# Optimization experiments

Hardware: AMD Instinct MI355X
Metric: run time of the kernel (lower is better)

Reference implementation:

```python
import jax, jax.numpy as jnp
import numpy as np

DT = 0.1       # integration step (ms)
TAU_M = 10.0   # membrane time constant
TAU_S = 5.0    # synaptic time constant
E_REV = 1.0    # synaptic reversal potential
G_MAX = 1.0    # synaptic conductance scale
P, N, E, B, T = 8, 2048, 16, 4, 128


def setup_inputs() -> dict:
    key = jax.random.key(0)
    k_src, k_tgt, k_w, k_win = jax.random.split(key, 4)
    t_seq = jnp.arange(B * T, dtype=jnp.float32).reshape(B, T) * DT  # [B,T] times in ms
    src = jax.random.randint(k_src, (E,), 0, P, dtype=jnp.int32)
    tgt = jax.random.randint(k_tgt, (E,), 0, P, dtype=jnp.int32)
    W = jax.random.normal(k_w, (E, N, N), jnp.float32) * (1.0 / np.sqrt(N))
    W_in = jax.random.normal(k_win, (N, N), jnp.float32) * (1.0 / np.sqrt(N))
    v0 = jnp.zeros((P, B, N), jnp.float32)      # population states
    s0 = jnp.zeros((E, B, N), jnp.float32)      # recurrent synapse states
    s_in0 = jnp.zeros((B, N), jnp.float32)      # input synapse state
    return dict(t_seq=t_seq, W=W, W_in=W_in, v0=v0, s0=s0, s_in0=s_in0, src=src, tgt=tgt)


def _input_rate(t, n):
    # InputPopulation: firing rate is a pure function of time t, per-unit phase.
    phase = jnp.arange(n, dtype=jnp.float32) * (2.0 * jnp.pi / n)
    return 0.5 * (1.0 + jnp.sin(2.0 * jnp.pi * t[:, None] / 100.0 + phase[None, :]))  # [B,n]


def _simulate(t_seq, W, W_in, v0, s0, s_in0, src, tgt):
    n_pop = v0.shape[0]

    def step(carry, t):  # t: [B] current time
        v, s, s_in, err = carry
        rates = jax.nn.sigmoid(v)                      # [P,B,N] firing rates
        # --- synapse message passing: gather pre rates, dense projection ---
        pre = rates[src]                               # [E,B,N]
        drive = jnp.einsum('ebi,eij->ebj', pre, W)     # [E,B,N]
        s_new = s + DT * (-s / TAU_S + drive)          # exponential synapse state
        # --- input population synapse (pre rate is a function of t) ---
        rate_in = _input_rate(t, v.shape[-1])          # [B,N]
        s_in_new = s_in + DT * (-s_in / TAU_S + rate_in @ W_in)
        # --- conductance-based currents scattered into target populations ---
        post_v = v[tgt]                                # [E,B,N]
        I_e = G_MAX * s_new * (E_REV - post_v)
        g_e = G_MAX * s_new
        I_sum = jax.ops.segment_sum(I_e, tgt, num_segments=n_pop)  # [P,B,N]
        g_sum = jax.ops.segment_sum(g_e, tgt, num_segments=n_pop)
        I_in = G_MAX * s_in_new * (E_REV - v[0])
        I_sum = I_sum.at[0].add(I_in)
        g_sum = g_sum.at[0].add(G_MAX * s_in_new)
        # --- Euler integrator step + stability error accumulation ---
        dv = (-v - g_sum * v + I_sum) / TAU_M
        v_new = v + DT * dv
        err_new = err + jnp.mean(jnp.abs(dv)) * DT
        return (v_new, s_new, s_in_new, err_new), jax.nn.sigmoid(v_new)

    init = (v0, s0, s_in0, jnp.zeros((), jnp.float32))
    (v_f, s_f, s_in_f, err), rates_seq = jax.lax.scan(step, init, t_seq.T)  # rates_seq: [T,P,B,N]
    firing_rates = jnp.transpose(rates_seq, (2, 0, 1, 3))  # [B,T,P,N]
    return firing_rates, err


def reference(t_seq, W, W_in, v0, s0, s_in0, src, tgt):
    return _simulate(t_seq, W, W_in, v0, s0, s_in0, src, tgt)
```

## Files before the change

### kernel.cpp

```cpp
#include <hip/hip_runtime.h>
#include <hip/hip_bf16.h>
#include <math.h>

#define DT_     0.1f
#define TAU_M_  10.0f
#define TAU_S_  5.0f
#define NP_     8
#define NN_     2048
#define NE_     16
#define NB_     4
#define NT_     128

#define CH_     16
#define IL_     128
#define NEDGE_  17

typedef __attribute__((ext_vector_type(8))) _Float16 half8;

template <typename T> struct V8;
template <> struct V8<float>    { typedef float    type __attribute__((ext_vector_type(8))); };
template <> struct V8<_Float16> { typedef _Float16 type __attribute__((ext_vector_type(8))); };

__device__ __forceinline__ float sigmoidf_(float x) {
  return 1.0f / (1.0f + expf(-x));
}

__global__ __launch_bounds__(256) void k_convert(
    const float* __restrict__ W, const float* __restrict__ W_in,
    _Float16* __restrict__ Wh) {
  size_t idx = ((size_t)blockIdx.x * 256 + threadIdx.x) * 8;
  const size_t lim = (size_t)NE_ * NN_ * NN_;
  const float* src = (idx < lim) ? (W + idx) : (W_in + (idx - lim));
  float4 a = *(const float4*)src;
  float4 b = *(const float4*)(src + 4);
  half8 h;
  h[0] = (_Float16)a.x; h[1] = (_Float16)a.y; h[2] = (_Float16)a.z; h[3] = (_Float16)a.w;
  h[4] = (_Float16)b.x; h[5] = (_Float16)b.y; h[6] = (_Float16)b.z; h[7] = (_Float16)b.w;
  *(half8*)(Wh + idx) = h;
}

__global__ __launch_bounds__(256) void k_init(
    const float* __restrict__ v0, const float* __restrict__ s0,
    const float* __restrict__ s_in0,
    float* __restrict__ v, float* __restrict__ s, float* __restrict__ s_in,
    float* __restrict__ rates, float* __restrict__ errpart) {
  int idx = blockIdx.x * 256 + threadIdx.x;
  if (idx < NE_ * NB_ * NN_) s[idx] = s0[idx];
  if (idx < NP_ * NB_ * NN_) {
    float vv = v0[idx];
    v[idx] = vv;
    rates[idx] = sigmoidf_(vv);
  }
  if (idx < NB_ * NN_) s_in[idx] = s_in0[idx];
  if (idx < 256) errpart[idx] = 0.0f;
}

template <typename WT>
__global__ __launch_bounds__(256) void k_stepA(
    const WT* __restrict__ Wall, const WT* __restrict__ Win,
    const float* __restrict__ rates, const float* __restrict__ t_seq,
    const int* __restrict__ src, float* __restrict__ part, int step) {
  const int e   = blockIdx.x;
  const int ch  = blockIdx.y;
  const int tid = threadIdx.x;

  __shared__ float pre[NB_][IL_];
  const int i0 = ch * IL_;

  for (int k = tid; k < NB_ * IL_; k += 256) {
    int b  = k >> 7;
    int il = k & (IL_ - 1);
    float val;
    if (e == 16) {
      float t = t_seq[b * NT_ + step];
      float phase = (float)(i0 + il) * (6.2831853071795864f / (float)NN_);
      val = 0.5f * (1.0f + sinf(0.062831853071795864f * t + phase));
    } else {
      val = rates[(src[e] * NB_ + b) * NN_ + (i0 + il)];
    }
    pre[b][il] = val;
  }
  __syncthreads();

  const WT* Wp = (e == 16) ? Win : (Wall + (size_t)e * NN_ * NN_);
  const int j = tid * 8;

  float acc[NB_][8] = {};
  typedef typename V8<WT>::type vec8;
#pragma unroll 4
  for (int il = 0; il < IL_; ++il) {
    vec8 w = *(const vec8*)(Wp + (size_t)(i0 + il) * NN_ + j);
    float wf[8];
#pragma unroll
    for (int k = 0; k < 8; ++k) wf[k] = (float)w[k];
#pragma unroll
    for (int b = 0; b < NB_; ++b) {
      float p = pre[b][il];
#pragma unroll
      for (int k = 0; k < 8; ++k) acc[b][k] += p * wf[k];
    }
  }

#pragma unroll
  for (int b = 0; b < NB_; ++b) {
    float4 o0 = {acc[b][0], acc[b][1], acc[b][2], acc[b][3]};
    float4 o1 = {acc[b][4], acc[b][5], acc[b][6], acc[b][7]};
    float* dst = part + (((size_t)ch * NEDGE_ + e) * NB_ + b) * NN_ + j;
    *(float4*)dst       = o0;
    *(float4*)(dst + 4) = o1;
  }
}

__global__ __launch_bounds__(256) void k_stepR(
    const float* __restrict__ part, float* __restrict__ s,
    float* __restrict__ s_in) {
  const int idx = blockIdx.x * 256 + threadIdx.x;
  const int e  = idx >> 12;
  const int r  = idx & 4095;
  const int b  = r >> 10;
  const int n  = (r & 1023) * 2;

  float2 acc = {0.0f, 0.0f};
#pragma unroll
  for (int c = 0; c < CH_; ++c) {
    float2 pv = *(const float2*)(part + (((size_t)c * NEDGE_ + e) * NB_ + b) * NN_ + n);
    acc.x += pv.x;
    acc.y += pv.y;
  }
  if (e == 16) {
    float2 sv = *(const float2*)(s_in + b * NN_ + n);
    sv.x += DT_ * (acc.x - sv.x * (1.0f / TAU_S_));
    sv.y += DT_ * (acc.y - sv.y * (1.0f / TAU_S_));
    *(float2*)(s_in + b * NN_ + n) = sv;
  } else {
    float* sp = s + ((size_t)e * NB_ + b) * NN_ + n;
    float2 sv = *(const float2*)sp;
    sv.x += DT_ * (acc.x - sv.x * (1.0f / TAU_S_));
    sv.y += DT_ * (acc.y - sv.y * (1.0f / TAU_S_));
    *(float2*)sp = sv;
  }
}

__global__ __launch_bounds__(256) void k_stepB(
    const float* __restrict__ s, const float* __restrict__ s_in,
    const int* __restrict__ tgt,
    float* __restrict__ v, float* __restrict__ rates,
    float* __restrict__ errpart, float* __restrict__ out, int step) {
  const int idx = blockIdx.x * 256 + threadIdx.x;
  const int p = idx >> 13;
  const int b = (idx >> 11) & (NB_ - 1);
  const int n = idx & (NN_ - 1);

  float S = 0.0f;
#pragma unroll
  for (int e = 0; e < NE_; ++e) {
    if (tgt[e] == p) S += s[((size_t)e * NB_ + b) * NN_ + n];
  }
  if (p == 0) S += s_in[b * NN_ + n];

  float* vp = v + ((size_t)p * NB_ + b) * NN_ + n;
  float vv = *vp;
  float I  = S * (1.0f - vv);
  float dv = (-vv - S * vv + I) * (1.0f / TAU_M_);
  float vn = vv + DT_ * dv;
  *vp = vn;
  float rr = sigmoidf_(vn);
  rates[((size_t)p * NB_ + b) * NN_ + n] = rr;
  out[(((size_t)b * NT_ + step) * NP_ + p) * NN_ + n] = rr;

  __shared__ float red[256];
  red[threadIdx.x] = fabsf(dv);
  __syncthreads();
  for (int w = 128; w > 0; w >>= 1) {
    if (threadIdx.x < w) red[threadIdx.x] += red[threadIdx.x + w];
    __syncthreads();
  }
  if (threadIdx.x == 0) {
    errpart[blockIdx.x] += red[0] * (DT_ / (float)(NP_ * NB_ * NN_));
  }
}

__global__ void k_final(const float* __restrict__ errpart,
                        float* __restrict__ out_err) {
  if (threadIdx.x == 0) {
    float sum = 0.0f;
    for (int i = 0; i < 256; ++i) sum += errpart[i];
    *out_err = sum;
  }
}

extern "C" void kernel_launch(void* const* d_in, const int* in_sizes, int n_in,
                              void* d_out, int out_size, void* d_ws, size_t ws_size,
                              hipStream_t stream) {
  const float* t_seq = (const float*)d_in[0];
  const float* W     = (const float*)d_in[1];
  const float* W_in  = (const float*)d_in[2];
  const float* v0    = (const float*)d_in[3];
  const float* s0    = (const float*)d_in[4];
  const float* s_in0 = (const float*)d_in[5];
  const int*   src   = (const int*)d_in[6];
  const int*   tgt   = (const int*)d_in[7];
  float* out = (float*)d_out;

  const size_t WH_ELEMS = (size_t)NEDGE_ * NN_ * NN_;
  const size_t PART_F   = (size_t)CH_ * NEDGE_ * NB_ * NN_;
  const size_t STATE_F  = 65536 + 131072 + 8192 + 65536 + 256;
  const size_t NEED_H   = WH_ELEMS * sizeof(_Float16) + (PART_F + STATE_F) * sizeof(float);
  const bool useHalf = ws_size >= NEED_H;

  _Float16* Wh;
  float* part;
  if (useHalf) {
    Wh   = (_Float16*)d_ws;
    part = (float*)(Wh + WH_ELEMS);
  } else {
    Wh   = nullptr;
    part = (float*)d_ws;
  }
  float* v       = part + PART_F;
  float* s       = v + NP_ * NB_ * NN_;
  float* s_in    = s + NE_ * NB_ * NN_;
  float* rates   = s_in + NB_ * NN_;
  float* errpart = rates + NP_ * NB_ * NN_;

  if (useHalf) {
    hipLaunchKernelGGL(k_convert, dim3((unsigned)(WH_ELEMS / (8 * 256))), dim3(256),
                       0, stream, W, W_in, Wh);
  }
  hipLaunchKernelGGL(k_init, dim3(512), dim3(256), 0, stream,
                     v0, s0, s_in0, v, s, s_in, rates, errpart);

  for (int t = 0; t < NT_; ++t) {
    if (useHalf) {
      hipLaunchKernelGGL(k_stepA<_Float16>, dim3(NEDGE_, CH_), dim3(256), 0, stream,
                         Wh, Wh + (size_t)NE_ * NN_ * NN_, rates, t_seq, src, part, t);
    } else {
      hipLaunchKernelGGL(k_stepA<float>, dim3(NEDGE_, CH_), dim3(256), 0, stream,
                         W, W_in, rates, t_seq, src, part, t);
    }
    hipLaunchKernelGGL(k_stepR, dim3(272), dim3(256), 0, stream, part, s, s_in);
    hipLaunchKernelGGL(k_stepB, dim3(256), dim3(256), 0, stream,
                       s, s_in, tgt, v, rates, errpart, out, t);
  }

  hipLaunchKernelGGL(k_final, dim3(1), dim3(64), 0, stream,
                     errpart, out + (size_t)NB_ * NT_ * NP_ * NN_);
}
```

Before: 4.180 ms.

## Split GEMV into more chunks and store partial sums in fp16

```diff
diff --git a/kernel.cpp b/kernel.cpp
--- a/kernel.cpp
+++ b/kernel.cpp
@@ -11,15 +11,16 @@
 #define NB_     4
 #define NT_     128
 
-#define CH_     16
-#define IL_     128
+#define CH_     32
+#define IL_     64
 #define NEDGE_  17
 
 typedef __attribute__((ext_vector_type(8))) _Float16 half8;
+typedef __attribute__((ext_vector_type(8))) float    float8;
 
 template <typename T> struct V8;
-template <> struct V8<float>    { typedef float    type __attribute__((ext_vector_type(8))); };
-template <> struct V8<_Float16> { typedef _Float16 type __attribute__((ext_vector_type(8))); };
+template <> struct V8<float>    { typedef float8 type; };
+template <> struct V8<_Float16> { typedef half8  type; };
 
 __device__ __forceinline__ float sigmoidf_(float x) {
   return 1.0f / (1.0f + expf(-x));
@@ -59,7 +60,7 @@
 __global__ __launch_bounds__(256) void k_stepA(
     const WT* __restrict__ Wall, const WT* __restrict__ Win,
     const float* __restrict__ rates, const float* __restrict__ t_seq,
-    const int* __restrict__ src, float* __restrict__ part, int step) {
+    const int* __restrict__ src, _Float16* __restrict__ part, int step) {
   const int e   = blockIdx.x;
   const int ch  = blockIdx.y;
   const int tid = threadIdx.x;
@@ -67,9 +68,9 @@
   __shared__ float pre[NB_][IL_];
   const int i0 = ch * IL_;
 
-  for (int k = tid; k < NB_ * IL_; k += 256) {
-    int b  = k >> 7;
-    int il = k & (IL_ - 1);
+  if (tid < NB_ * IL_) {
+    int b  = tid >> 6;
+    int il = tid & (IL_ - 1);
     float val;
     if (e == 16) {
       float t = t_seq[b * NT_ + step];
@@ -87,7 +88,7 @@
 
   float acc[NB_][8] = {};
   typedef typename V8<WT>::type vec8;
-#pragma unroll 4
+#pragma unroll 8
   for (int il = 0; il < IL_; ++il) {
     vec8 w = *(const vec8*)(Wp + (size_t)(i0 + il) * NN_ + j);
     float wf[8];
@@ -103,42 +104,43 @@
 
 #pragma unroll
   for (int b = 0; b < NB_; ++b) {
-    float4 o0 = {acc[b][0], acc[b][1], acc[b][2], acc[b][3]};
-    float4 o1 = {acc[b][4], acc[b][5], acc[b][6], acc[b][7]};
-    float* dst = part + (((size_t)ch * NEDGE_ + e) * NB_ + b) * NN_ + j;
-    *(float4*)dst       = o0;
-    *(float4*)(dst + 4) = o1;
+    half8 o;
+#pragma unroll
+    for (int k = 0; k < 8; ++k) o[k] = (_Float16)acc[b][k];
+    *(half8*)(part + (((size_t)ch * NEDGE_ + e) * NB_ + b) * NN_ + j) = o;
   }
 }
 
 __global__ __launch_bounds__(256) void k_stepR(
-    const float* __restrict__ part, float* __restrict__ s,
+    const _Float16* __restrict__ part, float* __restrict__ s,
     float* __restrict__ s_in) {
   const int idx = blockIdx.x * 256 + threadIdx.x;
-  const int e  = idx >> 12;
-  const int r  = idx & 4095;
-  const int b  = r >> 10;
-  const int n  = (r & 1023) * 2;
-
-  float2 acc = {0.0f, 0.0f};
+  const int e  = idx >> 10;
+  const int r  = idx & 1023;
+  const int b  = r >> 8;
+  const int n  = (r & 255) * 8;
+
+  float acc[8] = {};
 #pragma unroll
   for (int c = 0; c < CH_; ++c) {
-    float2 pv = *(const float2*)(part + (((size_t)c * NEDGE_ + e) * NB_ + b) * NN_ + n);
-    acc.x += pv.x;
-    acc.y += pv.y;
-  }
-  if (e == 16) {
-    float2 sv = *(const float2*)(s_in + b * NN_ + n);
-    sv.x += DT_ * (acc.x - sv.x * (1.0f / TAU_S_));
-    sv.y += DT_ * (acc.y - sv.y * (1.0f / TAU_S_));
-    *(float2*)(s_in + b * NN_ + n) = sv;
-  } else {
-    float* sp = s + ((size_t)e * NB_ + b) * NN_ + n;
-    float2 sv = *(const float2*)sp;
-    sv.x += DT_ * (acc.x - sv.x * (1.0f / TAU_S_));
-    sv.y += DT_ * (acc.y - sv.y * (1.0f / TAU_S_));
-    *(float2*)sp = sv;
-  }
+    half8 pv = *(const half8*)(part + (((size_t)c * NEDGE_ + e) * NB_ + b) * NN_ + n);
+#pragma unroll
+    for (int k = 0; k < 8; ++k) acc[k] += (float)pv[k];
+  }
+
+  float* sp = (e == 16) ? (s_in + b * NN_ + n) : (s + ((size_t)e * NB_ + b) * NN_ + n);
+  float4 s0 = *(const float4*)sp;
+  float4 s1 = *(const float4*)(sp + 4);
+  s0.x += DT_ * (acc[0] - s0.x * (1.0f / TAU_S_));
+  s0.y += DT_ * (acc[1] - s0.y * (1.0f / TAU_S_));
+  s0.z += DT_ * (acc[2] - s0.z * (1.0f / TAU_S_));
+  s0.w += DT_ * (acc[3] - s0.w * (1.0f / TAU_S_));
+  s1.x += DT_ * (acc[4] - s1.x * (1.0f / TAU_S_));
+  s1.y += DT_ * (acc[5] - s1.y * (1.0f / TAU_S_));
+  s1.z += DT_ * (acc[6] - s1.z * (1.0f / TAU_S_));
+  s1.w += DT_ * (acc[7] - s1.w * (1.0f / TAU_S_));
+  *(float4*)sp       = s0;
+  *(float4*)(sp + 4) = s1;
 }
 
 __global__ __launch_bounds__(256) void k_stepB(
@@ -151,10 +153,14 @@
   const int b = (idx >> 11) & (NB_ - 1);
   const int n = idx & (NN_ - 1);
 
+  int tg[NE_];
+#pragma unroll
+  for (int e = 0; e < NE_; ++e) tg[e] = tgt[e];
+
   float S = 0.0f;
 #pragma unroll
   for (int e = 0; e < NE_; ++e) {
-    if (tgt[e] == p) S += s[((size_t)e * NB_ + b) * NN_ + n];
+    if (tg[e] == p) S += s[((size_t)e * NB_ + b) * NN_ + n];
   }
   if (p == 0) S += s_in[b * NN_ + n];
 
@@ -166,7 +172,7 @@
   *vp = vn;
   float rr = sigmoidf_(vn);
   rates[((size_t)p * NB_ + b) * NN_ + n] = rr;
-  out[(((size_t)b * NT_ + step) * NP_ + p) * NN_ + n] = rr;
+  __builtin_nontemporal_store(rr, out + (((size_t)b * NT_ + step) * NP_ + p) * NN_ + n);
 
   __shared__ float red[256];
   red[threadIdx.x] = fabsf(dv);
@@ -203,21 +209,21 @@
   float* out = (float*)d_out;
 
   const size_t WH_ELEMS = (size_t)NEDGE_ * NN_ * NN_;
-  const size_t PART_F   = (size_t)CH_ * NEDGE_ * NB_ * NN_;
+  const size_t PART_H   = (size_t)CH_ * NEDGE_ * NB_ * NN_;
   const size_t STATE_F  = 65536 + 131072 + 8192 + 65536 + 256;
-  const size_t NEED_H   = WH_ELEMS * sizeof(_Float16) + (PART_F + STATE_F) * sizeof(float);
+  const size_t NEED_H   = (WH_ELEMS + PART_H) * sizeof(_Float16) + STATE_F * sizeof(float);
   const bool useHalf = ws_size >= NEED_H;
 
   _Float16* Wh;
-  float* part;
+  _Float16* part;
   if (useHalf) {
     Wh   = (_Float16*)d_ws;
-    part = (float*)(Wh + WH_ELEMS);
+    part = Wh + WH_ELEMS;
   } else {
     Wh   = nullptr;
-    part = (float*)d_ws;
-  }
-  float* v       = part + PART_F;
+    part = (_Float16*)d_ws;
+  }
+  float* v       = (float*)(part + PART_H);
   float* s       = v + NP_ * NB_ * NN_;
   float* s_in    = s + NE_ * NB_ * NN_;
   float* rates   = s_in + NB_ * NN_;
@@ -238,7 +244,7 @@
       hipLaunchKernelGGL(k_stepA<float>, dim3(NEDGE_, CH_), dim3(256), 0, stream,
                          W, W_in, rates, t_seq, src, part, t);
     }
-    hipLaunchKernelGGL(k_stepR, dim3(272), dim3(256), 0, stream, part, s, s_in);
+    hipLaunchKernelGGL(k_stepR, dim3(68), dim3(256), 0, stream, part, s, s_in);
     hipLaunchKernelGGL(k_stepB, dim3(256), dim3(256), 0, stream,
                        s, s_in, tgt, v, rates, errpart, out, t);
   }
```

New measurement: 4.375 ms. 1.05x slower.
